# Kernel optimization log

Measured on AMD Instinct MI355X. Metric: run time of the kernel, lower is better.

Reference implementation:

```python
import jax, jax.numpy as jnp
import numpy as np

B, T, C = 4, 2048, 1024
H = 16
D = C // H  # head_dim = 64


def setup_inputs() -> dict:
    key = jax.random.key(0)
    ks = jax.random.split(key, 6)
    s = 1.0 / np.sqrt(C)
    x = jax.random.normal(ks[0], (B, T, C), dtype=jnp.float32)
    Wq = jax.random.normal(ks[1], (C, C), dtype=jnp.float32) * s
    Wk = jax.random.normal(ks[2], (C, C), dtype=jnp.float32) * s
    Wv = jax.random.normal(ks[3], (C, C), dtype=jnp.float32) * s
    Wo = jax.random.normal(ks[4], (C, C), dtype=jnp.float32) * s
    bo = jnp.zeros((C,), dtype=jnp.float32)
    # causal mask, 1 = attend, 0 = masked (masked_fill(mask==0, -inf))
    mask = jnp.broadcast_to(jnp.tril(jnp.ones((T, T), dtype=jnp.int32)), (B, T, T))
    return {"x": x, "mask": mask, "Wq": Wq, "Wk": Wk, "Wv": Wv, "Wo": Wo, "bo": bo}


def reference(x, mask, Wq, Wk, Wv, Wo, bo):
    Bx, Tx, Cx = x.shape
    # projections; nn.Linear computes x @ W.T, here W is stored as (C, C) applied as x @ W
    Q = (x @ Wq).reshape(Bx, Tx, H, D).transpose(0, 2, 1, 3)  # (B,H,T,D)
    K = (x @ Wk).reshape(Bx, Tx, H, D).transpose(0, 2, 1, 3)
    V = (x @ Wv).reshape(Bx, Tx, H, D).transpose(0, 2, 1, 3)
    scores = jnp.einsum('bhqd,bhkd->bhqk', Q, K) / jnp.sqrt(jnp.float32(D))
    scores = jnp.where(mask[:, None, :, :] == 0, -jnp.inf, scores)
    attn = jax.nn.softmax(scores, axis=-1)
    ctx = jnp.einsum('bhqk,bhkd->bhqd', attn, V)  # (B,H,T,D)
    ctx = ctx.transpose(0, 2, 1, 3).reshape(Bx, Tx, Cx)
    return ctx @ Wo + bo
```

## Files before the change

### kernel.cpp

```cpp
#include <hip/hip_runtime.h>
#include <hip/hip_bf16.h>


#define B_  4
#define T_  2048
#define C_  1024
#define H_  16
#define D_  64
#define M_  (B_*T_)

#define LOG2E 1.4426950408889634f

using bf16x8 = __attribute__((ext_vector_type(8))) short;
using f32x4  = __attribute__((ext_vector_type(4))) float;
using u16x4  = __attribute__((ext_vector_type(4))) unsigned short;

__device__ __forceinline__ unsigned short f2bf(float f) {
  union { float f; unsigned u; } cv; cv.f = f;
  unsigned u = cv.u;
  u += 0x7fffu + ((u >> 16) & 1u);
  return (unsigned short)(u >> 16);
}

__device__ __forceinline__ unsigned cvt_pk_bf16(float lo, float hi) {
  unsigned r;
  asm("v_cvt_pk_bf16_f32 %0, %1, %2" : "=v"(r) : "v"(lo), "v"(hi));
  return r;
}

__device__ __forceinline__ float exp2fast(float x) {
#if __has_builtin(__builtin_amdgcn_exp2f)
  return __builtin_amdgcn_exp2f(x);
#else
  return exp2f(x);
#endif
}

__device__ __forceinline__ void lds_load16(void* lds, const void* g) {
  __builtin_amdgcn_global_load_lds(
      (const __attribute__((address_space(1))) unsigned int*)g,
      (__attribute__((address_space(3))) unsigned int*)lds,
      16, 0, 0);
}

__global__ __launch_bounds__(256) void conv_x_kernel(
    const float* __restrict__ x, unsigned short* __restrict__ xb) {
  int i = blockIdx.x * 256 + threadIdx.x;
  const float4* xv = (const float4*)x;
  float4 a = xv[i * 2 + 0];
  float4 b = xv[i * 2 + 1];
  using u16x8 = __attribute__((ext_vector_type(8))) unsigned short;
  u16x8 o;
  o[0]=f2bf(a.x); o[1]=f2bf(a.y); o[2]=f2bf(a.z); o[3]=f2bf(a.w);
  o[4]=f2bf(b.x); o[5]=f2bf(b.y); o[6]=f2bf(b.z); o[7]=f2bf(b.w);
  *(u16x8*)&xb[(size_t)i * 8] = o;
}

__global__ __launch_bounds__(256) void conv_wt_kernel(
    const float* __restrict__ W0, const float* __restrict__ W1,
    const float* __restrict__ W2, const float* __restrict__ W3,
    unsigned short* __restrict__ WT) {
  __shared__ float tile[64][65];
  const float* W = (blockIdx.z == 0) ? W0 : (blockIdx.z == 1) ? W1
                 : (blockIdx.z == 2) ? W2 : W3;
  unsigned short* o = WT + (size_t)blockIdx.z * C_ * C_;
  const int k0 = blockIdx.y * 64, n0 = blockIdx.x * 64;
  const int tr = threadIdx.x >> 6;
  const int tc = threadIdx.x & 63;
#pragma unroll
  for (int i = 0; i < 16; ++i) {
    int k = tr + i * 4;
    tile[k][tc] = W[(size_t)(k0 + k) * C_ + n0 + tc];
  }
  __syncthreads();
#pragma unroll
  for (int i = 0; i < 16; ++i) {
    int n = tr + i * 4;
    o[(size_t)(n0 + n) * C_ + k0 + tc] = f2bf(tile[tc][n]);
  }
}

template <int EPI>
__global__ __launch_bounds__(256) void gemm128(
    const unsigned short* __restrict__ A, const unsigned short* __restrict__ BT,
    void* __restrict__ out, const float* __restrict__ bias, int K) {
  __shared__ unsigned short As[128][32];
  __shared__ unsigned short Bs[128][32];

  const int tid  = threadIdx.x;
  const int wid  = tid >> 6, lane = tid & 63;
  const int wr   = wid >> 1, wc = wid & 1;
  const int fr   = lane & 15, fq = lane >> 4;
  const int bid  = blockIdx.y * gridDim.x + blockIdx.x;
  const int xcd  = bid & 7, ii = bid >> 3;
  const int bm   = xcd + 8 * (ii & 7);
  const int bn   = ii >> 3;

  const unsigned short* aP = A  + (size_t)(bm * 128 + wid * 32 + (lane >> 2)) * K + (lane & 3) * 8;
  const unsigned short* bP = BT + (size_t)(bn * 128 + wid * 32 + (lane >> 2)) * K + (lane & 3) * 8;
  unsigned short* asB = &As[wid * 32][0];
  unsigned short* bsB = &Bs[wid * 32][0];

  f32x4 acc[4][4] = {};

  for (int k0 = 0; k0 < K; k0 += 32) {
    lds_load16(asB,           aP + k0);
    lds_load16(asB + 16 * 32, aP + (size_t)16 * K + k0);
    lds_load16(bsB,           bP + k0);
    lds_load16(bsB + 16 * 32, bP + (size_t)16 * K + k0);
    __syncthreads();

    bf16x8 af[4], bfr[4];
#pragma unroll
    for (int mi = 0; mi < 4; ++mi)
      af[mi] = *(const bf16x8*)&As[wr * 64 + mi * 16 + fr][fq * 8];
#pragma unroll
    for (int ni = 0; ni < 4; ++ni)
      bfr[ni] = *(const bf16x8*)&Bs[wc * 64 + ni * 16 + fr][fq * 8];
#pragma unroll
    for (int mi = 0; mi < 4; ++mi)
#pragma unroll
      for (int ni = 0; ni < 4; ++ni)
        acc[mi][ni] = __builtin_amdgcn_mfma_f32_16x16x32_bf16(
            af[mi], bfr[ni], acc[mi][ni], 0, 0, 0);
    __syncthreads();
  }

  if (EPI == 0) {
    unsigned short* o = (unsigned short*)out;
#pragma unroll
    for (int mi = 0; mi < 4; ++mi) {
      int m  = bm * 128 + wr * 64 + mi * 16 + fq * 4;
      int b  = m >> 11;
      int t0 = m & 2047;
#pragma unroll
      for (int ni = 0; ni < 4; ++ni) {
        int n = bn * 128 + wc * 64 + ni * 16 + fr;
        int mat = n >> 10;
        int nc  = n & 1023;
        int h = nc >> 6, d = nc & 63;
        float sc_ = (mat == 0) ? (0.125f * LOG2E) : 1.0f;
        size_t base = (size_t)mat * ((size_t)M_ * C_) + ((size_t)(b * H_ + h) << 17) + d;
#pragma unroll
        for (int r = 0; r < 4; ++r)
          o[base + (size_t)(t0 + r) * D_] = f2bf(acc[mi][ni][r] * sc_);
      }
    }
  } else {
    float* o = (float*)out;
#pragma unroll
    for (int mi = 0; mi < 4; ++mi) {
      int m = bm * 128 + wr * 64 + mi * 16 + fq * 4;
#pragma unroll
      for (int ni = 0; ni < 4; ++ni) {
        int n = bn * 128 + wc * 64 + ni * 16 + fr;
        float bv = bias[n];
#pragma unroll
        for (int r = 0; r < 4; ++r)
          o[(size_t)(m + r) * C_ + n] = acc[mi][ni][r] + bv;
      }
    }
  }
}

#define KSTR 72
__global__ __launch_bounds__(256) void attn_kernel(
    const unsigned short* __restrict__ Qg, const unsigned short* __restrict__ Kg,
    const unsigned short* __restrict__ Vg, unsigned short* __restrict__ ctx) {
  __shared__ __align__(16) unsigned short Ks[2][64][KSTR];
  __shared__ __align__(16) unsigned short VTs[2][64][KSTR];

  const int tid = threadIdx.x, wid = tid >> 6, lane = tid & 63;
  const int fr = lane & 15, fq = lane >> 4;

  const int bid = blockIdx.x;
  const int xcd = bid & 7, j = bid >> 3;
  const int bh = xcd * 8 + (j & 7);
  const int qt = 15 - (j >> 3);
  const int b = bh >> 4, h = bh & 15;
  const size_t base = (size_t)bh * (T_ * D_);

  const int ksr = tid >> 2, ksc = tid & 3;
  const int kpr = ((ksr >> 5) & 1) * 32 + ((ksr >> 2) & 1) * 16 +
                  ((ksr >> 3) & 3) * 4 + (ksr & 3);
  const unsigned short* Kptr = Kg + base + (size_t)ksr * D_ + ksc * 8;
  const int vc = tid >> 5, vr_ = tid & 31;
  const unsigned short* Vptr = Vg + base + (size_t)(2 * vr_) * D_ + vc * 8;

  int4 kr0, kr1, va, vb;
  auto stage_load = [&](int kv) {
    const unsigned short* kp = Kptr + (size_t)kv * D_;
    kr0 = *(const int4*)kp;
    kr1 = *(const int4*)(kp + 32);
    const unsigned short* vp = Vptr + (size_t)kv * D_;
    va = *(const int4*)vp;
    vb = *(const int4*)(vp + D_);
  };
  auto stage_write = [&](int nb) {
    *(int4*)&Ks[nb][kpr][ksc * 8]       = kr0;
    *(int4*)&Ks[nb][kpr][(ksc + 4) * 8] = kr1;
    const unsigned short* pa = (const unsigned short*)&va;
    const unsigned short* pb = (const unsigned short*)&vb;
#pragma unroll
    for (int i = 0; i < 8; ++i) {
      unsigned w = (unsigned)pa[i] | ((unsigned)pb[i] << 16);
      *(unsigned*)&VTs[nb][vc * 8 + i][2 * vr_] = w;
    }
  };

  stage_load(0);
  stage_write(0);

  const int qbase = qt * 128;

  bf16x8 qf[2][2];
#pragma unroll
  for (int x = 0; x < 2; ++x)
#pragma unroll
    for (int t = 0; t < 2; ++t)
      qf[x][t] = *(const bf16x8*)
          &Qg[base + (size_t)(qbase + 64 * x + wid * 16 + fr) * D_ + t * 32 + fq * 8];

  f32x4 acc[2][4] = {};
  float m_run[2] = {-__builtin_inff(), -__builtin_inff()};
  float l_run[2] = {0.f, 0.f};

  const int nsteps = 2 * qt + 2;
  int kv0 = 0;
  for (int s = 0; s < nsteps; ++s) {
    const int  cur = s & 1;
    const bool have_next = (s + 1 < nsteps);

    __syncthreads();
    if (have_next) stage_load(kv0 + 64);

    bf16x8 kf[8];
#pragma unroll
    for (int nt = 0; nt < 4; ++nt)
#pragma unroll
      for (int t = 0; t < 2; ++t)
        kf[nt * 2 + t] = *(const bf16x8*)&Ks[cur][nt * 16 + fr][t * 32 + fq * 8];

    bf16x8 pf[2][2];
#pragma unroll
    for (int x = 0; x < 2; ++x) {
      f32x4 sv[4];
      __builtin_amdgcn_s_setprio(1);
#pragma unroll
      for (int nt = 0; nt < 4; ++nt) {
        f32x4 sa = {};
        sa = __builtin_amdgcn_mfma_f32_16x16x32_bf16(kf[nt * 2 + 0], qf[x][0], sa, 0, 0, 0);
        sa = __builtin_amdgcn_mfma_f32_16x16x32_bf16(kf[nt * 2 + 1], qf[x][1], sa, 0, 0, 0);
        sv[nt] = sa;
      }
      __builtin_amdgcn_s_setprio(0);

      float mt = -__builtin_inff();
      if (kv0 >= qbase + 64 * x) {
        const int qi = qbase + 64 * x + wid * 16 + fr;
#pragma unroll
        for (int nt = 0; nt < 4; ++nt)
#pragma unroll
          for (int r = 0; r < 4; ++r) {
            int kvi = kv0 + 32 * (nt >> 1) + 8 * fq + 4 * (nt & 1) + r;
            float v = sv[nt][r];
            if (kvi > qi) v = -__builtin_inff();
            sv[nt][r] = v;
            mt = fmaxf(mt, v);
          }
      } else {
#pragma unroll
        for (int nt = 0; nt < 4; ++nt)
          mt = fmaxf(mt, fmaxf(fmaxf(sv[nt][0], sv[nt][1]),
                               fmaxf(sv[nt][2], sv[nt][3])));
      }
      mt = fmaxf(mt, __shfl_xor(mt, 16));
      mt = fmaxf(mt, __shfl_xor(mt, 32));

      if (__any(mt > m_run[x] + 8.0f)) {
        float mn = fmaxf(m_run[x], mt);
        float c  = exp2fast(m_run[x] - mn);
        m_run[x] = mn;
#pragma unroll
        for (int dt = 0; dt < 4; ++dt) acc[x][dt] *= c;
        l_run[x] *= c;
      }

      float lsum = 0.f;
      int pw[8];
#pragma unroll
      for (int nt = 0; nt < 4; ++nt) {
        float p0 = exp2fast(sv[nt][0] - m_run[x]);
        float p1 = exp2fast(sv[nt][1] - m_run[x]);
        float p2 = exp2fast(sv[nt][2] - m_run[x]);
        float p3 = exp2fast(sv[nt][3] - m_run[x]);
        lsum += (p0 + p1) + (p2 + p3);
        pw[(nt >> 1) * 4 + (nt & 1) * 2 + 0] = (int)cvt_pk_bf16(p0, p1);
        pw[(nt >> 1) * 4 + (nt & 1) * 2 + 1] = (int)cvt_pk_bf16(p2, p3);
      }
      l_run[x] += lsum;

#pragma unroll
      for (int t = 0; t < 2; ++t) {
        int4 v4 = {pw[t * 4 + 0], pw[t * 4 + 1], pw[t * 4 + 2], pw[t * 4 + 3]};
        pf[x][t] = __builtin_bit_cast(bf16x8, v4);
      }
    }

    __builtin_amdgcn_s_setprio(1);
#pragma unroll
    for (int t = 0; t < 2; ++t)
#pragma unroll
      for (int dt = 0; dt < 4; ++dt) {
        bf16x8 vf = *(const bf16x8*)&VTs[cur][dt * 16 + fr][t * 32 + fq * 8];
        acc[0][dt] = __builtin_amdgcn_mfma_f32_16x16x32_bf16(vf, pf[0][t], acc[0][dt], 0, 0, 0);
        acc[1][dt] = __builtin_amdgcn_mfma_f32_16x16x32_bf16(vf, pf[1][t], acc[1][dt], 0, 0, 0);
      }
    __builtin_amdgcn_s_setprio(0);

    if (have_next) stage_write(cur ^ 1);
    kv0 += 64;
  }

#pragma unroll
  for (int x = 0; x < 2; ++x) {
    float l = l_run[x];
    l += __shfl_xor(l, 16);
    l += __shfl_xor(l, 32);
    float linv = 1.0f / l;
    unsigned short* orow =
        ctx + (size_t)(b * T_ + qbase + 64 * x + wid * 16 + fr) * C_ + h * D_;
#pragma unroll
    for (int dt = 0; dt < 4; ++dt) {
      u16x4 o;
#pragma unroll
      for (int r = 0; r < 4; ++r) o[r] = f2bf(acc[x][dt][r] * linv);
      *(u16x4*)&orow[dt * 16 + fq * 4] = o;
    }
  }
}

extern "C" void kernel_launch(void* const* d_in, const int* in_sizes, int n_in,
                              void* d_out, int out_size, void* d_ws, size_t ws_size,
                              hipStream_t stream) {
  const float* x  = (const float*)d_in[0];
  const float* Wq = (const float*)d_in[2];
  const float* Wk = (const float*)d_in[3];
  const float* Wv = (const float*)d_in[4];
  const float* Wo = (const float*)d_in[5];
  const float* bo = (const float*)d_in[6];

  unsigned short* xb  = (unsigned short*)d_ws;
  unsigned short* wqt = xb  + (size_t)M_ * C_;
  unsigned short* wot = wqt + (size_t)3 * C_ * C_;
  unsigned short* Qb  = wot + (size_t)C_ * C_;
  unsigned short* ctxb = xb;

  conv_x_kernel<<<4096, 256, 0, stream>>>(x, xb);
  conv_wt_kernel<<<dim3(16, 16, 4), 256, 0, stream>>>(Wq, Wk, Wv, Wo, wqt);

  gemm128<0><<<dim3(24, M_ / 128), 256, 0, stream>>>(xb, wqt, Qb, nullptr, C_);

  attn_kernel<<<dim3(1024), 256, 0, stream>>>(
      Qb, Qb + (size_t)M_ * C_, Qb + (size_t)2 * M_ * C_, ctxb);

  gemm128<1><<<dim3(8, M_ / 128), 256, 0, stream>>>(ctxb, wot, d_out, bo, C_);
}
```

Baseline: 191.0 us.

## Enlarge attention Q tile to 256 rows with 8 warps, split K/V staging across warps

The attention kernel now uses 512-thread blocks, each covering 256 query rows (32 per warp), with half as many blocks launched. Each K/V tile staged in shared memory is therefore reused by twice as many query rows, roughly halving global K/V traffic and staging work per query. Staging is also split so that warps 0-3 load and transpose V while warps 4-7 load K, each thread holding two registers instead of four. The trade-off is coarser causal work imbalance across 512 blocks, fewer blocks to fill the GPU, and more waves per barrier.

```diff
diff --git a/kernel.cpp b/kernel.cpp
--- a/kernel.cpp
+++ b/kernel.cpp
@@ -164,7 +164,7 @@
 }
 
 #define KSTR 72
-__global__ __launch_bounds__(256) void attn_kernel(
+__global__ __launch_bounds__(512) void attn_kernel(
     const unsigned short* __restrict__ Qg, const unsigned short* __restrict__ Kg,
     const unsigned short* __restrict__ Vg, unsigned short* __restrict__ ctx) {
   __shared__ __align__(16) unsigned short Ks[2][64][KSTR];
@@ -176,42 +176,49 @@
   const int bid = blockIdx.x;
   const int xcd = bid & 7, j = bid >> 3;
   const int bh = xcd * 8 + (j & 7);
-  const int qt = 15 - (j >> 3);
+  const int qt = 7 - (j >> 3);
   const int b = bh >> 4, h = bh & 15;
   const size_t base = (size_t)bh * (T_ * D_);
 
-  const int ksr = tid >> 2, ksc = tid & 3;
+  const int vc = (tid & 255) >> 5, vr_ = tid & 31;
+  const int kt = tid & 255, ksr = kt >> 2, ksc = kt & 3;
   const int kpr = ((ksr >> 5) & 1) * 32 + ((ksr >> 2) & 1) * 16 +
                   ((ksr >> 3) & 3) * 4 + (ksr & 3);
   const unsigned short* Kptr = Kg + base + (size_t)ksr * D_ + ksc * 8;
-  const int vc = tid >> 5, vr_ = tid & 31;
   const unsigned short* Vptr = Vg + base + (size_t)(2 * vr_) * D_ + vc * 8;
 
-  int4 kr0, kr1, va, vb;
+  int4 sa_, sb_;
   auto stage_load = [&](int kv) {
-    const unsigned short* kp = Kptr + (size_t)kv * D_;
-    kr0 = *(const int4*)kp;
-    kr1 = *(const int4*)(kp + 32);
-    const unsigned short* vp = Vptr + (size_t)kv * D_;
-    va = *(const int4*)vp;
-    vb = *(const int4*)(vp + D_);
+    if (wid < 4) {
+      const unsigned short* vp = Vptr + (size_t)kv * D_;
+      sa_ = *(const int4*)vp;
+      sb_ = *(const int4*)(vp + D_);
+    } else {
+      const unsigned short* kp = Kptr + (size_t)kv * D_;
+      sa_ = *(const int4*)kp;
+      sb_ = *(const int4*)(kp + 32);
+    }
   };
   auto stage_write = [&](int nb) {
-    *(int4*)&Ks[nb][kpr][ksc * 8]       = kr0;
-    *(int4*)&Ks[nb][kpr][(ksc + 4) * 8] = kr1;
-    const unsigned short* pa = (const unsigned short*)&va;
-    const unsigned short* pb = (const unsigned short*)&vb;
-#pragma unroll
-    for (int i = 0; i < 8; ++i) {
-      unsigned w = (unsigned)pa[i] | ((unsigned)pb[i] << 16);
-      *(unsigned*)&VTs[nb][vc * 8 + i][2 * vr_] = w;
+    if (wid < 4) {
+      const unsigned short* pa = (const unsigned short*)&sa_;
+      const unsigned short* pb = (const unsigned short*)&sb_;
+#pragma unroll
+      for (int i = 0; i < 8; ++i) {
+        unsigned w = (unsigned)pa[i] | ((unsigned)pb[i] << 16);
+        *(unsigned*)&VTs[nb][vc * 8 + i][2 * vr_] = w;
+      }
+    } else {
+      *(int4*)&Ks[nb][kpr][ksc * 8]       = sa_;
+      *(int4*)&Ks[nb][kpr][(ksc + 4) * 8] = sb_;
     }
   };
 
   stage_load(0);
   stage_write(0);
 
-  const int qbase = qt * 128;
+  const int qbase = qt * 256;
+  const int qrow = qbase + wid * 32;
 
   bf16x8 qf[2][2];
 #pragma unroll
@@ -219,13 +226,13 @@
 #pragma unroll
     for (int t = 0; t < 2; ++t)
       qf[x][t] = *(const bf16x8*)
-          &Qg[base + (size_t)(qbase + 64 * x + wid * 16 + fr) * D_ + t * 32 + fq * 8];
+          &Qg[base + (size_t)(qrow + 16 * x + fr) * D_ + t * 32 + fq * 8];
 
   f32x4 acc[2][4] = {};
   float m_run[2] = {-__builtin_inff(), -__builtin_inff()};
   float l_run[2] = {0.f, 0.f};
 
-  const int nsteps = 2 * qt + 2;
+  const int nsteps = 4 * qt + 4;
   int kv0 = 0;
   for (int s = 0; s < nsteps; ++s) {
     const int  cur = s & 1;
@@ -255,9 +262,10 @@
       }
       __builtin_amdgcn_s_setprio(0);
 
+      const int qrx = qrow + 16 * x;
       float mt = -__builtin_inff();
-      if (kv0 >= qbase + 64 * x) {
-        const int qi = qbase + 64 * x + wid * 16 + fr;
+      if (kv0 + 63 > qrx) {
+        const int qi = qrx + fr;
 #pragma unroll
         for (int nt = 0; nt < 4; ++nt)
 #pragma unroll
@@ -329,7 +337,7 @@
     l += __shfl_xor(l, 32);
     float linv = 1.0f / l;
     unsigned short* orow =
-        ctx + (size_t)(b * T_ + qbase + 64 * x + wid * 16 + fr) * C_ + h * D_;
+        ctx + (size_t)(b * T_ + qrow + 16 * x + fr) * C_ + h * D_;
 #pragma unroll
     for (int dt = 0; dt < 4; ++dt) {
       u16x4 o;
@@ -361,7 +369,7 @@
 
   gemm128<0><<<dim3(24, M_ / 128), 256, 0, stream>>>(xb, wqt, Qb, nullptr, C_);
 
-  attn_kernel<<<dim3(1024), 256, 0, stream>>>(
+  attn_kernel<<<dim3(512), 512, 0, stream>>>(
       Qb, Qb + (size_t)M_ * C_, Qb + (size_t)2 * M_ * C_, ctxb);
 
   gemm128<1><<<dim3(8, M_ / 128), 256, 0, stream>>>(ctxb, wot, d_out, bo, C_);
```

New measurement: 177.5 us. 7.1% less time.
